# Optimization experiments

Hardware: AMD Instinct MI355X
Metric: run time of the kernel (lower is better)

Reference implementation:

```python
import jax, jax.numpy as jnp
import numpy as np

NB_HEADS = 4
EMBED_DIM = 128
EPS = 1e-06


def setup_inputs() -> dict:
    key = jax.random.key(0)
    ks = jax.random.split(key, 9)
    B, R, C, E = 2, 64, 2048, 128
    s = 1.0 / np.sqrt(E)
    inp = {
        "input": jax.random.normal(ks[0], (B, R, C, E), dtype=jnp.float32),
        # weights stored as (in, out); torch Linear applies x @ W.T + b, equivalent here
        "Wq": jax.random.normal(ks[1], (E, E), dtype=jnp.float32) * s,
        "bq": jax.random.normal(ks[2], (E,), dtype=jnp.float32) * 0.01,
        "Wk": jax.random.normal(ks[3], (E, E), dtype=jnp.float32) * s,
        "bk": jax.random.normal(ks[4], (E,), dtype=jnp.float32) * 0.01,
        "Wv": jax.random.normal(ks[5], (E, E), dtype=jnp.float32) * s,
        "bv": jax.random.normal(ks[6], (E,), dtype=jnp.float32) * 0.01,
        "Wo": jax.random.normal(ks[7], (E, E), dtype=jnp.float32) * s,
        "bo": jax.random.normal(ks[8], (E,), dtype=jnp.float32) * 0.01,
    }
    return inp


def reference(input, Wq, bq, Wk, bk, Wv, bv, Wo, bo):
    B, R, C, E = input.shape
    H = NB_HEADS
    Dh = E // H
    # projections, split into heads: (B, R, C, H, Dh)
    q = (input @ Wq + bq).reshape(B, R, C, H, Dh)
    k = (input @ Wk + bk).reshape(B, R, C, H, Dh)
    v = (input @ Wv + bv).reshape(B, R, C, H, Dh)
    # elu+1 feature map
    q = jax.nn.elu(q) + 1.0
    k = jax.nn.elu(k) + 1.0
    # KtV: contract over col axis -> (B, R, H, Dh, Dh)
    KtV = jnp.einsum('brchd,brche->brhde', k, v)
    # normalizer: q . sum_c(k) -> (B, R, C, H)
    ksum = k.sum(axis=2)  # (B, R, H, Dh)
    Z = 1.0 / (jnp.einsum('brchd,brhd->brch', q, ksum) + EPS)
    # attention output: (B, R, C, H, Dh)
    out = jnp.einsum('brchd,brhde->brche', q, KtV) * Z[..., None]
    out = out.reshape(B, R, C, E)
    return out @ Wo + bo
```

## Files before the change

kernel.cpp:

```cpp
#include <hip/hip_runtime.h>

#define DEVINL __device__ __forceinline__

typedef __attribute__((ext_vector_type(8))) __bf16 bf16x8;
typedef __attribute__((ext_vector_type(4))) __bf16 bf16x4;
typedef __attribute__((ext_vector_type(4))) float f32x4;

DEVINL f32x4 mfma16(bf16x8 a, bf16x8 b, f32x4 c) {
  return __builtin_amdgcn_mfma_f32_16x16x32_bf16(a, b, c, 0, 0, 0);
}

DEVINL bf16x8 loadWfrag(const float* __restrict__ W, int kb, int n) {
  bf16x8 f;
#pragma unroll
  for (int j = 0; j < 8; ++j) f[j] = (__bf16)W[(kb + j) * 128 + n];
  return f;
}

__global__ __launch_bounds__(256, 2)
void qkv_ktv_kernel(const float* __restrict__ X,
                    const float* __restrict__ Wq, const float* __restrict__ bq,
                    const float* __restrict__ Wk, const float* __restrict__ bk,
                    const float* __restrict__ Wv, const float* __restrict__ bv,
                    __bf16* __restrict__ Qout,
                    float* __restrict__ ktvWs, float* __restrict__ ksumWs)
{
  __shared__ __bf16 Xs[64 * 136];
  __shared__ __bf16 Kt[128 * 72];
  __shared__ __bf16 Vt[128 * 72];

  const int tid  = threadIdx.x;
  const int lane = tid & 63;
  const int w    = tid >> 6;
  const int l15  = lane & 15;
  const int quad = lane >> 4;
  const int s     = blockIdx.x >> 2;
  const int chunk = blockIdx.x & 3;
  const int tokc0 = chunk * 512;
  const float* Xseq = X + (size_t)s * 2048 * 128;

  bf16x8 wkF[2][4], wvF[2][4], wqF[2][4];
#pragma unroll
  for (int nt = 0; nt < 2; ++nt) {
    const int n = w * 32 + nt * 16 + l15;
#pragma unroll
    for (int kk = 0; kk < 4; ++kk) {
      const int kb = kk * 32 + quad * 8;
      wkF[nt][kk] = loadWfrag(Wk, kb, n);
      wvF[nt][kk] = loadWfrag(Wv, kb, n);
      wqF[nt][kk] = loadWfrag(Wq, kb, n);
    }
  }
  float bkr[2], bvr[2], bqr[2][4];
#pragma unroll
  for (int nt = 0; nt < 2; ++nt) {
    bkr[nt] = bk[w * 32 + nt * 16 + l15];
    bvr[nt] = bv[w * 32 + nt * 16 + l15];
#pragma unroll
    for (int r = 0; r < 4; ++r)
      bqr[nt][r] = bq[w * 32 + nt * 16 + quad * 4 + r];
  }

  f32x4 accT[2][2] = {};
  float ksumAcc[2] = {0.f, 0.f};

  for (int t = 0; t < 8; ++t) {
    const float* Xtile = Xseq + (size_t)(tokc0 + t * 64) * 128;
    __syncthreads();
#pragma unroll
    for (int i = 0; i < 8; ++i) {
      const int flat = tid + i * 256;
      const int row = flat >> 5;
      const int c4  = (flat & 31) * 4;
      const float4 v = *(const float4*)(Xtile + row * 128 + c4);
      bf16x4 b4;
      b4[0] = (__bf16)v.x; b4[1] = (__bf16)v.y;
      b4[2] = (__bf16)v.z; b4[3] = (__bf16)v.w;
      *(bf16x4*)(&Xs[row * 136 + c4]) = b4;
    }
    __syncthreads();

#pragma unroll
    for (int mt = 0; mt < 4; ++mt) {
      f32x4 aK[2] = {}, aV[2] = {};
#pragma unroll
      for (int kk = 0; kk < 4; ++kk) {
        const bf16x8 ax = *(const bf16x8*)(&Xs[(mt * 16 + l15) * 136 + kk * 32 + quad * 8]);
        aK[0] = mfma16(ax, wkF[0][kk], aK[0]);
        aK[1] = mfma16(ax, wkF[1][kk], aK[1]);
        aV[0] = mfma16(ax, wvF[0][kk], aV[0]);
        aV[1] = mfma16(ax, wvF[1][kk], aV[1]);
      }
#pragma unroll
      for (int nt = 0; nt < 2; ++nt) {
        const int e    = w * 32 + nt * 16 + l15;
        const int tokb = mt * 16 + quad * 4;
        bf16x4 kq, vq;
        float ks = 0.f;
#pragma unroll
        for (int r = 0; r < 4; ++r) {
          float kv = aK[nt][r] + bkr[nt];
          kv = (kv > 0.f) ? (kv + 1.f) : __expf(kv);
          ks += kv;
          kq[r] = (__bf16)kv;
          vq[r] = (__bf16)(aV[nt][r] + bvr[nt]);
        }
        ksumAcc[nt] += ks;
        *(bf16x4*)(&Kt[e * 72 + tokb]) = kq;
        *(bf16x4*)(&Vt[e * 72 + tokb]) = vq;
      }
    }

#pragma unroll
    for (int ntq = 0; ntq < 4; ++ntq) {
      f32x4 aQ[2] = {};
#pragma unroll
      for (int kk = 0; kk < 4; ++kk) {
        const bf16x8 bx = *(const bf16x8*)(&Xs[(ntq * 16 + l15) * 136 + kk * 32 + quad * 8]);
        aQ[0] = mfma16(wqF[0][kk], bx, aQ[0]);
        aQ[1] = mfma16(wqF[1][kk], bx, aQ[1]);
      }
      const int tok = tokc0 + t * 64 + ntq * 16 + l15;
      __bf16* qrow = Qout + ((size_t)s * 2048 + tok) * 128;
#pragma unroll
      for (int mt = 0; mt < 2; ++mt) {
        bf16x4 qq;
#pragma unroll
        for (int r = 0; r < 4; ++r) {
          float qv = aQ[mt][r] + bqr[mt][r];
          qv = (qv > 0.f) ? (qv + 1.f) : __expf(qv);
          qq[r] = (__bf16)qv;
        }
        *(bf16x4*)(qrow + w * 32 + mt * 16 + quad * 4) = qq;
      }
    }
    __syncthreads();

#pragma unroll
    for (int kk = 0; kk < 2; ++kk) {
      bf16x8 aF[2], bF[2];
#pragma unroll
      for (int dt = 0; dt < 2; ++dt)
        aF[dt] = *(const bf16x8*)(&Kt[(w * 32 + dt * 16 + l15) * 72 + kk * 32 + quad * 8]);
#pragma unroll
      for (int et = 0; et < 2; ++et)
        bF[et] = *(const bf16x8*)(&Vt[(w * 32 + et * 16 + l15) * 72 + kk * 32 + quad * 8]);
#pragma unroll
      for (int dt = 0; dt < 2; ++dt)
#pragma unroll
        for (int et = 0; et < 2; ++et)
          accT[dt][et] = mfma16(aF[dt], bF[et], accT[dt][et]);
    }
  }

  float* ktvH = ktvWs + ((size_t)s * 4 + w) * 1024;
#pragma unroll
  for (int dt = 0; dt < 2; ++dt)
#pragma unroll
    for (int et = 0; et < 2; ++et)
#pragma unroll
      for (int r = 0; r < 4; ++r)
        atomicAdd(&ktvH[(dt * 16 + quad * 4 + r) * 32 + et * 16 + l15], accT[dt][et][r]);

#pragma unroll
  for (int nt = 0; nt < 2; ++nt) {
    float v2 = ksumAcc[nt];
    v2 += __shfl_down(v2, 32);
    v2 += __shfl_down(v2, 16);
    if (quad == 0)
      atomicAdd(&ksumWs[s * 128 + w * 32 + nt * 16 + l15], v2);
  }
}

__global__ __launch_bounds__(256, 2)
void attn_out_kernel(const __bf16* __restrict__ Qin,
                     const float* __restrict__ ktvWs, const float* __restrict__ ksumWs,
                     const float* __restrict__ Wo, const float* __restrict__ bo,
                     float* __restrict__ Out)
{
  __shared__ __bf16 Qs[64 * 136];
  __shared__ __bf16 A2s[64 * 136];
  __shared__ float ksums[128];
  __shared__ float Zs[64 * 4];

  const int tid  = threadIdx.x;
  const int lane = tid & 63;
  const int w    = tid >> 6;
  const int l15  = lane & 15;
  const int quad = lane >> 4;
  const int s     = blockIdx.x >> 2;
  const int chunk = blockIdx.x & 3;

  if (tid < 128) ksums[tid] = ksumWs[s * 128 + tid];

  const float* ktvH = ktvWs + ((size_t)s * 4 + w) * 1024;
  bf16x8 aKtv[2];
#pragma unroll
  for (int mt = 0; mt < 2; ++mt)
#pragma unroll
    for (int j = 0; j < 8; ++j)
      aKtv[mt][j] = (__bf16)ktvH[(quad * 8 + j) * 32 + mt * 16 + l15];

  bf16x8 woF[2][4];
  float bor[2];
#pragma unroll
  for (int nt = 0; nt < 2; ++nt) {
    const int n = w * 32 + nt * 16 + l15;
    bor[nt] = bo[n];
#pragma unroll
    for (int kk = 0; kk < 4; ++kk)
      woF[nt][kk] = loadWfrag(Wo, kk * 32 + quad * 8, n);
  }
  __syncthreads();

  for (int t = 0; t < 8; ++t) {
    const int tok0 = chunk * 512 + t * 64;
    const __bf16* Qtile = Qin + ((size_t)s * 2048 + tok0) * 128;
    __syncthreads();
#pragma unroll
    for (int i = 0; i < 4; ++i) {
      const int c = tid + i * 256;
      const int row = c >> 4, cc = (c & 15) * 8;
      *(bf16x8*)(&Qs[row * 136 + cc]) = *(const bf16x8*)(Qtile + row * 128 + cc);
    }
    __syncthreads();
    {
      const int tok = tid >> 2, h = tid & 3;
      float dot = 0.f;
      const __bf16* qrow = &Qs[tok * 136 + h * 32];
      const float* ksrow = &ksums[h * 32];
#pragma unroll
      for (int j = 0; j < 32; ++j) dot += (float)qrow[j] * ksrow[j];
      Zs[tok * 4 + h] = 1.f / (dot + 1e-6f);
    }
    __syncthreads();
#pragma unroll
    for (int ntq = 0; ntq < 4; ++ntq) {
      const bf16x8 bq8 = *(const bf16x8*)(&Qs[(ntq * 16 + l15) * 136 + w * 32 + quad * 8]);
      f32x4 acc[2] = {};
      acc[0] = mfma16(aKtv[0], bq8, acc[0]);
      acc[1] = mfma16(aKtv[1], bq8, acc[1]);
      const int tokRow = ntq * 16 + l15;
      const float z = Zs[tokRow * 4 + w];
#pragma unroll
      for (int mt = 0; mt < 2; ++mt) {
        bf16x4 a4;
#pragma unroll
        for (int r = 0; r < 4; ++r) a4[r] = (__bf16)(acc[mt][r] * z);
        *(bf16x4*)(&A2s[tokRow * 136 + w * 32 + mt * 16 + quad * 4]) = a4;
      }
    }
    __syncthreads();
#pragma unroll
    for (int mt = 0; mt < 4; ++mt) {
      f32x4 acc[2] = {};
#pragma unroll
      for (int kk = 0; kk < 4; ++kk) {
        const bf16x8 aa = *(const bf16x8*)(&A2s[(mt * 16 + l15) * 136 + kk * 32 + quad * 8]);
        acc[0] = mfma16(aa, woF[0][kk], acc[0]);
        acc[1] = mfma16(aa, woF[1][kk], acc[1]);
      }
      const int tokb = tok0 + mt * 16 + quad * 4;
      float* orow = Out + ((size_t)s * 2048 + tokb) * 128;
#pragma unroll
      for (int nt = 0; nt < 2; ++nt) {
        const int n = w * 32 + nt * 16 + l15;
#pragma unroll
        for (int r = 0; r < 4; ++r)
          orow[(size_t)r * 128 + n] = acc[nt][r] + bor[nt];
      }
    }
  }
}

extern "C" void kernel_launch(void* const* d_in, const int* in_sizes, int n_in,
                              void* d_out, int out_size, void* d_ws, size_t ws_size,
                              hipStream_t stream) {
  const float* X  = (const float*)d_in[0];
  const float* Wq = (const float*)d_in[1];
  const float* bq = (const float*)d_in[2];
  const float* Wk = (const float*)d_in[3];
  const float* bk = (const float*)d_in[4];
  const float* Wv = (const float*)d_in[5];
  const float* bv = (const float*)d_in[6];
  const float* Wo = (const float*)d_in[7];
  const float* bo = (const float*)d_in[8];
  float* Out = (float*)d_out;

  const size_t Q_BYTES    = (size_t)128 * 2048 * 128 * 2;
  const size_t KTV_BYTES  = (size_t)128 * 4 * 32 * 32 * 4;
  const size_t KSUM_BYTES = (size_t)128 * 128 * 4;
  __bf16* Qws   = (__bf16*)d_ws;
  float* ktvWs  = (float*)((char*)d_ws + Q_BYTES);
  float* ksumWs = (float*)((char*)d_ws + Q_BYTES + KTV_BYTES);

  hipMemsetAsync((char*)d_ws + Q_BYTES, 0, KTV_BYTES + KSUM_BYTES, stream);

  qkv_ktv_kernel<<<dim3(512), dim3(256), 0, stream>>>(
      X, Wq, bq, Wk, bk, Wv, bv, Qws, ktvWs, ksumWs);
  attn_out_kernel<<<dim3(512), dim3(256), 0, stream>>>(
      Qws, ktvWs, ksumWs, Wo, bo, Out);
}
```

Before: 310.5 us.

## Recompute Q in output kernel instead of materializing it, split grid finer

Moves the Q projection out of the first kernel and into the output kernel, which rereads X and recomputes Q rather than writing and then reading a bf16 Q buffer in global memory. The normalizer is computed in registers with shuffles, and Q and A2 share one LDS buffer. Both kernels now launch 1024 blocks of 256 tokens with higher occupancy hints, and the first kernel register-prefetches the next X tile. The trade is a second fp32 read of X in place of the bf16 Q write and read, plus more blocks doing atomic adds into KtV.

```diff
diff --git a/kernel.cpp b/kernel.cpp
--- a/kernel.cpp
+++ b/kernel.cpp
@@ -17,13 +17,11 @@
   return f;
 }
 
-__global__ __launch_bounds__(256, 2)
-void qkv_ktv_kernel(const float* __restrict__ X,
-                    const float* __restrict__ Wq, const float* __restrict__ bq,
-                    const float* __restrict__ Wk, const float* __restrict__ bk,
-                    const float* __restrict__ Wv, const float* __restrict__ bv,
-                    __bf16* __restrict__ Qout,
-                    float* __restrict__ ktvWs, float* __restrict__ ksumWs)
+__global__ __launch_bounds__(256, 3)
+void kv_ktv_kernel(const float* __restrict__ X,
+                   const float* __restrict__ Wk, const float* __restrict__ bk,
+                   const float* __restrict__ Wv, const float* __restrict__ bv,
+                   float* __restrict__ ktvWs, float* __restrict__ ksumWs)
 {
   __shared__ __bf16 Xs[64 * 136];
   __shared__ __bf16 Kt[128 * 72];
@@ -34,12 +32,18 @@
   const int w    = tid >> 6;
   const int l15  = lane & 15;
   const int quad = lane >> 4;
-  const int s     = blockIdx.x >> 2;
-  const int chunk = blockIdx.x & 3;
-  const int tokc0 = chunk * 512;
-  const float* Xseq = X + (size_t)s * 2048 * 128;
-
-  bf16x8 wkF[2][4], wvF[2][4], wqF[2][4];
+  const int s     = blockIdx.x >> 3;
+  const int chunk = blockIdx.x & 7;
+  const float* Xc = X + ((size_t)s * 2048 + chunk * 256) * 128;
+
+  float4 xst[8];
+#pragma unroll
+  for (int i = 0; i < 8; ++i) {
+    const int flat = tid + i * 256;
+    xst[i] = *(const float4*)(Xc + (flat >> 5) * 128 + (flat & 31) * 4);
+  }
+
+  bf16x8 wkF[2][4], wvF[2][4];
 #pragma unroll
   for (int nt = 0; nt < 2; ++nt) {
     const int n = w * 32 + nt * 16 + l15;
@@ -48,35 +52,37 @@
       const int kb = kk * 32 + quad * 8;
       wkF[nt][kk] = loadWfrag(Wk, kb, n);
       wvF[nt][kk] = loadWfrag(Wv, kb, n);
-      wqF[nt][kk] = loadWfrag(Wq, kb, n);
-    }
-  }
-  float bkr[2], bvr[2], bqr[2][4];
+    }
+  }
+  float bkr[2], bvr[2];
 #pragma unroll
   for (int nt = 0; nt < 2; ++nt) {
     bkr[nt] = bk[w * 32 + nt * 16 + l15];
     bvr[nt] = bv[w * 32 + nt * 16 + l15];
-#pragma unroll
-    for (int r = 0; r < 4; ++r)
-      bqr[nt][r] = bq[w * 32 + nt * 16 + quad * 4 + r];
   }
 
   f32x4 accT[2][2] = {};
   float ksumAcc[2] = {0.f, 0.f};
 
-  for (int t = 0; t < 8; ++t) {
-    const float* Xtile = Xseq + (size_t)(tokc0 + t * 64) * 128;
+  for (int t = 0; t < 4; ++t) {
     __syncthreads();
 #pragma unroll
     for (int i = 0; i < 8; ++i) {
       const int flat = tid + i * 256;
       const int row = flat >> 5;
       const int c4  = (flat & 31) * 4;
-      const float4 v = *(const float4*)(Xtile + row * 128 + c4);
       bf16x4 b4;
-      b4[0] = (__bf16)v.x; b4[1] = (__bf16)v.y;
-      b4[2] = (__bf16)v.z; b4[3] = (__bf16)v.w;
+      b4[0] = (__bf16)xst[i].x; b4[1] = (__bf16)xst[i].y;
+      b4[2] = (__bf16)xst[i].z; b4[3] = (__bf16)xst[i].w;
       *(bf16x4*)(&Xs[row * 136 + c4]) = b4;
+    }
+    if (t < 3) {
+      const float* Xn = Xc + (t + 1) * 64 * 128;
+#pragma unroll
+      for (int i = 0; i < 8; ++i) {
+        const int flat = tid + i * 256;
+        xst[i] = *(const float4*)(Xn + (flat >> 5) * 128 + (flat & 31) * 4);
+      }
     }
     __syncthreads();
 
@@ -112,31 +118,6 @@
     }
 
 #pragma unroll
-    for (int ntq = 0; ntq < 4; ++ntq) {
-      f32x4 aQ[2] = {};
-#pragma unroll
-      for (int kk = 0; kk < 4; ++kk) {
-        const bf16x8 bx = *(const bf16x8*)(&Xs[(ntq * 16 + l15) * 136 + kk * 32 + quad * 8]);
-        aQ[0] = mfma16(wqF[0][kk], bx, aQ[0]);
-        aQ[1] = mfma16(wqF[1][kk], bx, aQ[1]);
-      }
-      const int tok = tokc0 + t * 64 + ntq * 16 + l15;
-      __bf16* qrow = Qout + ((size_t)s * 2048 + tok) * 128;
-#pragma unroll
-      for (int mt = 0; mt < 2; ++mt) {
-        bf16x4 qq;
-#pragma unroll
-        for (int r = 0; r < 4; ++r) {
-          float qv = aQ[mt][r] + bqr[mt][r];
-          qv = (qv > 0.f) ? (qv + 1.f) : __expf(qv);
-          qq[r] = (__bf16)qv;
-        }
-        *(bf16x4*)(qrow + w * 32 + mt * 16 + quad * 4) = qq;
-      }
-    }
-    __syncthreads();
-
-#pragma unroll
     for (int kk = 0; kk < 2; ++kk) {
       bf16x8 aF[2], bF[2];
 #pragma unroll
@@ -172,27 +153,43 @@
   }
 }
 
-__global__ __launch_bounds__(256, 2)
-void attn_out_kernel(const __bf16* __restrict__ Qin,
+__global__ __launch_bounds__(256, 4)
+void attn_out_kernel(const float* __restrict__ X,
+                     const float* __restrict__ Wq, const float* __restrict__ bq,
                      const float* __restrict__ ktvWs, const float* __restrict__ ksumWs,
                      const float* __restrict__ Wo, const float* __restrict__ bo,
                      float* __restrict__ Out)
 {
-  __shared__ __bf16 Qs[64 * 136];
-  __shared__ __bf16 A2s[64 * 136];
-  __shared__ float ksums[128];
-  __shared__ float Zs[64 * 4];
+  __shared__ __bf16 Xs[64 * 136];
+  __shared__ __bf16 QA2s[64 * 136];
 
   const int tid  = threadIdx.x;
   const int lane = tid & 63;
   const int w    = tid >> 6;
   const int l15  = lane & 15;
   const int quad = lane >> 4;
-  const int s     = blockIdx.x >> 2;
-  const int chunk = blockIdx.x & 3;
-
-  if (tid < 128) ksums[tid] = ksumWs[s * 128 + tid];
-
+  const int s     = blockIdx.x >> 3;
+  const int chunk = blockIdx.x & 7;
+  const float* Xc = X + ((size_t)s * 2048 + chunk * 256) * 128;
+  float* OutC = Out + ((size_t)s * 2048 + chunk * 256) * 128;
+
+  bf16x8 wqF[2][4], woF[2][4];
+  float bqr[2][4], bor[2], ksumr[2][4];
+#pragma unroll
+  for (int nt = 0; nt < 2; ++nt) {
+    const int n = w * 32 + nt * 16 + l15;
+#pragma unroll
+    for (int kk = 0; kk < 4; ++kk) {
+      wqF[nt][kk] = loadWfrag(Wq, kk * 32 + quad * 8, n);
+      woF[nt][kk] = loadWfrag(Wo, kk * 32 + quad * 8, n);
+    }
+    bor[nt] = bo[n];
+#pragma unroll
+    for (int r = 0; r < 4; ++r) {
+      bqr[nt][r]   = bq[w * 32 + nt * 16 + quad * 4 + r];
+      ksumr[nt][r] = ksumWs[s * 128 + w * 32 + nt * 16 + quad * 4 + r];
+    }
+  }
   const float* ktvH = ktvWs + ((size_t)s * 4 + w) * 1024;
   bf16x8 aKtv[2];
 #pragma unroll
@@ -201,67 +198,77 @@
     for (int j = 0; j < 8; ++j)
       aKtv[mt][j] = (__bf16)ktvH[(quad * 8 + j) * 32 + mt * 16 + l15];
 
-  bf16x8 woF[2][4];
-  float bor[2];
-#pragma unroll
-  for (int nt = 0; nt < 2; ++nt) {
-    const int n = w * 32 + nt * 16 + l15;
-    bor[nt] = bo[n];
-#pragma unroll
-    for (int kk = 0; kk < 4; ++kk)
-      woF[nt][kk] = loadWfrag(Wo, kk * 32 + quad * 8, n);
-  }
-  __syncthreads();
-
-  for (int t = 0; t < 8; ++t) {
-    const int tok0 = chunk * 512 + t * 64;
-    const __bf16* Qtile = Qin + ((size_t)s * 2048 + tok0) * 128;
-    __syncthreads();
-#pragma unroll
-    for (int i = 0; i < 4; ++i) {
-      const int c = tid + i * 256;
-      const int row = c >> 4, cc = (c & 15) * 8;
-      *(bf16x8*)(&Qs[row * 136 + cc]) = *(const bf16x8*)(Qtile + row * 128 + cc);
-    }
-    __syncthreads();
-    {
-      const int tok = tid >> 2, h = tid & 3;
+  for (int t = 0; t < 4; ++t) {
+    const float* Xt = Xc + t * 64 * 128;
+    __syncthreads();
+#pragma unroll
+    for (int i = 0; i < 8; ++i) {
+      const int flat = tid + i * 256;
+      const int row = flat >> 5;
+      const int c4  = (flat & 31) * 4;
+      const float4 v = *(const float4*)(Xt + row * 128 + c4);
+      bf16x4 b4;
+      b4[0] = (__bf16)v.x; b4[1] = (__bf16)v.y;
+      b4[2] = (__bf16)v.z; b4[3] = (__bf16)v.w;
+      *(bf16x4*)(&Xs[row * 136 + c4]) = b4;
+    }
+    __syncthreads();
+
+    float zreg[4];
+#pragma unroll
+    for (int ntq = 0; ntq < 4; ++ntq) {
+      f32x4 aQ[2] = {};
+#pragma unroll
+      for (int kk = 0; kk < 4; ++kk) {
+        const bf16x8 bx = *(const bf16x8*)(&Xs[(ntq * 16 + l15) * 136 + kk * 32 + quad * 8]);
+        aQ[0] = mfma16(wqF[0][kk], bx, aQ[0]);
+        aQ[1] = mfma16(wqF[1][kk], bx, aQ[1]);
+      }
       float dot = 0.f;
-      const __bf16* qrow = &Qs[tok * 136 + h * 32];
-      const float* ksrow = &ksums[h * 32];
-#pragma unroll
-      for (int j = 0; j < 32; ++j) dot += (float)qrow[j] * ksrow[j];
-      Zs[tok * 4 + h] = 1.f / (dot + 1e-6f);
-    }
-    __syncthreads();
+#pragma unroll
+      for (int mt = 0; mt < 2; ++mt) {
+        bf16x4 qq;
+#pragma unroll
+        for (int r = 0; r < 4; ++r) {
+          float qv = aQ[mt][r] + bqr[mt][r];
+          qv = (qv > 0.f) ? (qv + 1.f) : __expf(qv);
+          dot += qv * ksumr[mt][r];
+          qq[r] = (__bf16)qv;
+        }
+        *(bf16x4*)(&QA2s[(ntq * 16 + l15) * 136 + w * 32 + mt * 16 + quad * 4]) = qq;
+      }
+      dot += __shfl_xor(dot, 16);
+      dot += __shfl_xor(dot, 32);
+      zreg[ntq] = 1.f / (dot + 1e-6f);
+    }
+
 #pragma unroll
     for (int ntq = 0; ntq < 4; ++ntq) {
-      const bf16x8 bq8 = *(const bf16x8*)(&Qs[(ntq * 16 + l15) * 136 + w * 32 + quad * 8]);
+      const bf16x8 bq8 = *(const bf16x8*)(&QA2s[(ntq * 16 + l15) * 136 + w * 32 + quad * 8]);
       f32x4 acc[2] = {};
       acc[0] = mfma16(aKtv[0], bq8, acc[0]);
       acc[1] = mfma16(aKtv[1], bq8, acc[1]);
-      const int tokRow = ntq * 16 + l15;
-      const float z = Zs[tokRow * 4 + w];
+      const float z = zreg[ntq];
 #pragma unroll
       for (int mt = 0; mt < 2; ++mt) {
         bf16x4 a4;
 #pragma unroll
         for (int r = 0; r < 4; ++r) a4[r] = (__bf16)(acc[mt][r] * z);
-        *(bf16x4*)(&A2s[tokRow * 136 + w * 32 + mt * 16 + quad * 4]) = a4;
-      }
-    }
-    __syncthreads();
+        *(bf16x4*)(&QA2s[(ntq * 16 + l15) * 136 + w * 32 + mt * 16 + quad * 4]) = a4;
+      }
+    }
+    __syncthreads();
+
 #pragma unroll
     for (int mt = 0; mt < 4; ++mt) {
       f32x4 acc[2] = {};
 #pragma unroll
       for (int kk = 0; kk < 4; ++kk) {
-        const bf16x8 aa = *(const bf16x8*)(&A2s[(mt * 16 + l15) * 136 + kk * 32 + quad * 8]);
+        const bf16x8 aa = *(const bf16x8*)(&QA2s[(mt * 16 + l15) * 136 + kk * 32 + quad * 8]);
         acc[0] = mfma16(aa, woF[0][kk], acc[0]);
         acc[1] = mfma16(aa, woF[1][kk], acc[1]);
       }
-      const int tokb = tok0 + mt * 16 + quad * 4;
-      float* orow = Out + ((size_t)s * 2048 + tokb) * 128;
+      float* orow = OutC + (size_t)(t * 64 + mt * 16 + quad * 4) * 128;
 #pragma unroll
       for (int nt = 0; nt < 2; ++nt) {
         const int n = w * 32 + nt * 16 + l15;
@@ -287,17 +294,15 @@
   const float* bo = (const float*)d_in[8];
   float* Out = (float*)d_out;
 
-  const size_t Q_BYTES    = (size_t)128 * 2048 * 128 * 2;
   const size_t KTV_BYTES  = (size_t)128 * 4 * 32 * 32 * 4;
   const size_t KSUM_BYTES = (size_t)128 * 128 * 4;
-  __bf16* Qws   = (__bf16*)d_ws;
-  float* ktvWs  = (float*)((char*)d_ws + Q_BYTES);
-  float* ksumWs = (float*)((char*)d_ws + Q_BYTES + KTV_BYTES);
-
-  hipMemsetAsync((char*)d_ws + Q_BYTES, 0, KTV_BYTES + KSUM_BYTES, stream);
-
-  qkv_ktv_kernel<<<dim3(512), dim3(256), 0, stream>>>(
-      X, Wq, bq, Wk, bk, Wv, bv, Qws, ktvWs, ksumWs);
-  attn_out_kernel<<<dim3(512), dim3(256), 0, stream>>>(
-      Qws, ktvWs, ksumWs, Wo, bo, Out);
-}
+  float* ktvWs  = (float*)d_ws;
+  float* ksumWs = (float*)((char*)d_ws + KTV_BYTES);
+
+  hipMemsetAsync(d_ws, 0, KTV_BYTES + KSUM_BYTES, stream);
+
+  kv_ktv_kernel<<<dim3(1024), dim3(256), 0, stream>>>(
+      X, Wk, bk, Wv, bv, ktvWs, ksumWs);
+  attn_out_kernel<<<dim3(1024), dim3(256), 0, stream>>>(
+      X, Wq, bq, ktvWs, ksumWs, Wo, bo, Out);
+}
```

Result: slower. 439.0 us (+41.4%).

## Split sequences into 8 chunks with partial KtV buffers instead of atomics

Applied to the files above, without the earlier changes.

Doubles the grid to 1024 blocks of 256 tokens each and raises the launch-bounds occupancy target to 4 blocks per CU. Each block now writes its partial KtV and ksum to a private slot, and the output kernel reduces the 8 partials, which removes the memset and the global atomics. The KtV MFMA is interleaved with the K/V projection in 32-token halves using smaller LDS tiles, dropping one barrier per tile. The normalizer Z is computed in registers with shuffles instead of a separate LDS pass. In exchange, every output block re-reads and re-sums 8 partial tiles, and the higher occupancy target may cause register spills.

```diff
diff --git a/kernel.cpp b/kernel.cpp
--- a/kernel.cpp
+++ b/kernel.cpp
@@ -17,27 +17,27 @@
   return f;
 }
 
-__global__ __launch_bounds__(256, 2)
+__global__ __launch_bounds__(256, 4)
 void qkv_ktv_kernel(const float* __restrict__ X,
                     const float* __restrict__ Wq, const float* __restrict__ bq,
                     const float* __restrict__ Wk, const float* __restrict__ bk,
                     const float* __restrict__ Wv, const float* __restrict__ bv,
                     __bf16* __restrict__ Qout,
-                    float* __restrict__ ktvWs, float* __restrict__ ksumWs)
+                    float* __restrict__ ktvP, float* __restrict__ ksumP)
 {
   __shared__ __bf16 Xs[64 * 136];
-  __shared__ __bf16 Kt[128 * 72];
-  __shared__ __bf16 Vt[128 * 72];
+  __shared__ __bf16 Kt[128 * 40];
+  __shared__ __bf16 Vt[128 * 40];
 
   const int tid  = threadIdx.x;
   const int lane = tid & 63;
   const int w    = tid >> 6;
   const int l15  = lane & 15;
   const int quad = lane >> 4;
-  const int s     = blockIdx.x >> 2;
-  const int chunk = blockIdx.x & 3;
-  const int tokc0 = chunk * 512;
-  const float* Xseq = X + (size_t)s * 2048 * 128;
+  const int s     = blockIdx.x >> 3;
+  const int chunk = blockIdx.x & 7;
+  const int tokc0 = chunk * 256;
+  const float* Xc = X + ((size_t)s * 2048 + tokc0) * 128;
 
   bf16x8 wkF[2][4], wvF[2][4], wqF[2][4];
 #pragma unroll
@@ -64,8 +64,8 @@
   f32x4 accT[2][2] = {};
   float ksumAcc[2] = {0.f, 0.f};
 
-  for (int t = 0; t < 8; ++t) {
-    const float* Xtile = Xseq + (size_t)(tokc0 + t * 64) * 128;
+  for (int t = 0; t < 4; ++t) {
+    const float* Xtile = Xc + t * 64 * 128;
     __syncthreads();
 #pragma unroll
     for (int i = 0; i < 8; ++i) {
@@ -81,34 +81,50 @@
     __syncthreads();
 
 #pragma unroll
-    for (int mt = 0; mt < 4; ++mt) {
-      f32x4 aK[2] = {}, aV[2] = {};
-#pragma unroll
-      for (int kk = 0; kk < 4; ++kk) {
-        const bf16x8 ax = *(const bf16x8*)(&Xs[(mt * 16 + l15) * 136 + kk * 32 + quad * 8]);
-        aK[0] = mfma16(ax, wkF[0][kk], aK[0]);
-        aK[1] = mfma16(ax, wkF[1][kk], aK[1]);
-        aV[0] = mfma16(ax, wvF[0][kk], aV[0]);
-        aV[1] = mfma16(ax, wvF[1][kk], aV[1]);
-      }
-#pragma unroll
-      for (int nt = 0; nt < 2; ++nt) {
-        const int e    = w * 32 + nt * 16 + l15;
-        const int tokb = mt * 16 + quad * 4;
-        bf16x4 kq, vq;
-        float ks = 0.f;
-#pragma unroll
-        for (int r = 0; r < 4; ++r) {
-          float kv = aK[nt][r] + bkr[nt];
-          kv = (kv > 0.f) ? (kv + 1.f) : __expf(kv);
-          ks += kv;
-          kq[r] = (__bf16)kv;
-          vq[r] = (__bf16)(aV[nt][r] + bvr[nt]);
+    for (int half = 0; half < 2; ++half) {
+#pragma unroll
+      for (int mt2 = 0; mt2 < 2; ++mt2) {
+        const int mt = half * 2 + mt2;
+        f32x4 aK[2] = {}, aV[2] = {};
+#pragma unroll
+        for (int kk = 0; kk < 4; ++kk) {
+          const bf16x8 ax = *(const bf16x8*)(&Xs[(mt * 16 + l15) * 136 + kk * 32 + quad * 8]);
+          aK[0] = mfma16(ax, wkF[0][kk], aK[0]);
+          aK[1] = mfma16(ax, wkF[1][kk], aK[1]);
+          aV[0] = mfma16(ax, wvF[0][kk], aV[0]);
+          aV[1] = mfma16(ax, wvF[1][kk], aV[1]);
         }
-        ksumAcc[nt] += ks;
-        *(bf16x4*)(&Kt[e * 72 + tokb]) = kq;
-        *(bf16x4*)(&Vt[e * 72 + tokb]) = vq;
-      }
+#pragma unroll
+        for (int nt = 0; nt < 2; ++nt) {
+          const int e    = w * 32 + nt * 16 + l15;
+          const int tokb = mt2 * 16 + quad * 4;
+          bf16x4 kq, vq;
+          float ks = 0.f;
+#pragma unroll
+          for (int r = 0; r < 4; ++r) {
+            float kv = aK[nt][r] + bkr[nt];
+            kv = (kv > 0.f) ? (kv + 1.f) : __expf(kv);
+            ks += kv;
+            kq[r] = (__bf16)kv;
+            vq[r] = (__bf16)(aV[nt][r] + bvr[nt]);
+          }
+          ksumAcc[nt] += ks;
+          *(bf16x4*)(&Kt[e * 40 + tokb]) = kq;
+          *(bf16x4*)(&Vt[e * 40 + tokb]) = vq;
+        }
+      }
+      bf16x8 aF[2], bF[2];
+#pragma unroll
+      for (int dt = 0; dt < 2; ++dt)
+        aF[dt] = *(const bf16x8*)(&Kt[(w * 32 + dt * 16 + l15) * 40 + quad * 8]);
+#pragma unroll
+      for (int et = 0; et < 2; ++et)
+        bF[et] = *(const bf16x8*)(&Vt[(w * 32 + et * 16 + l15) * 40 + quad * 8]);
+#pragma unroll
+      for (int dt = 0; dt < 2; ++dt)
+#pragma unroll
+        for (int et = 0; et < 2; ++et)
+          accT[dt][et] = mfma16(aF[dt], bF[et], accT[dt][et]);
     }
 
 #pragma unroll
@@ -134,33 +150,16 @@
         *(bf16x4*)(qrow + w * 32 + mt * 16 + quad * 4) = qq;
       }
     }
-    __syncthreads();
-
-#pragma unroll
-    for (int kk = 0; kk < 2; ++kk) {
-      bf16x8 aF[2], bF[2];
-#pragma unroll
-      for (int dt = 0; dt < 2; ++dt)
-        aF[dt] = *(const bf16x8*)(&Kt[(w * 32 + dt * 16 + l15) * 72 + kk * 32 + quad * 8]);
-#pragma unroll
-      for (int et = 0; et < 2; ++et)
-        bF[et] = *(const bf16x8*)(&Vt[(w * 32 + et * 16 + l15) * 72 + kk * 32 + quad * 8]);
-#pragma unroll
-      for (int dt = 0; dt < 2; ++dt)
-#pragma unroll
-        for (int et = 0; et < 2; ++et)
-          accT[dt][et] = mfma16(aF[dt], bF[et], accT[dt][et]);
-    }
-  }
-
-  float* ktvH = ktvWs + ((size_t)s * 4 + w) * 1024;
+  }
+
+  float* kp = ktvP + ((size_t)blockIdx.x * 4 + w) * 1024;
 #pragma unroll
   for (int dt = 0; dt < 2; ++dt)
 #pragma unroll
     for (int et = 0; et < 2; ++et)
 #pragma unroll
       for (int r = 0; r < 4; ++r)
-        atomicAdd(&ktvH[(dt * 16 + quad * 4 + r) * 32 + et * 16 + l15], accT[dt][et][r]);
+        kp[(dt * 16 + quad * 4 + r) * 32 + et * 16 + l15] = accT[dt][et][r];
 
 #pragma unroll
   for (int nt = 0; nt < 2; ++nt) {
@@ -168,38 +167,48 @@
     v2 += __shfl_down(v2, 32);
     v2 += __shfl_down(v2, 16);
     if (quad == 0)
-      atomicAdd(&ksumWs[s * 128 + w * 32 + nt * 16 + l15], v2);
-  }
-}
-
-__global__ __launch_bounds__(256, 2)
+      ksumP[(size_t)blockIdx.x * 128 + w * 32 + nt * 16 + l15] = v2;
+  }
+}
+
+__global__ __launch_bounds__(256, 4)
 void attn_out_kernel(const __bf16* __restrict__ Qin,
-                     const float* __restrict__ ktvWs, const float* __restrict__ ksumWs,
+                     const float* __restrict__ ktvP, const float* __restrict__ ksumP,
                      const float* __restrict__ Wo, const float* __restrict__ bo,
                      float* __restrict__ Out)
 {
   __shared__ __bf16 Qs[64 * 136];
   __shared__ __bf16 A2s[64 * 136];
-  __shared__ float ksums[128];
-  __shared__ float Zs[64 * 4];
 
   const int tid  = threadIdx.x;
   const int lane = tid & 63;
   const int w    = tid >> 6;
   const int l15  = lane & 15;
   const int quad = lane >> 4;
-  const int s     = blockIdx.x >> 2;
-  const int chunk = blockIdx.x & 3;
-
-  if (tid < 128) ksums[tid] = ksumWs[s * 128 + tid];
-
-  const float* ktvH = ktvWs + ((size_t)s * 4 + w) * 1024;
+  const int s     = blockIdx.x >> 3;
+  const int chunk = blockIdx.x & 7;
+
+  const float* kpBase = ktvP + ((size_t)s * 8 * 4 + w) * 1024;
   bf16x8 aKtv[2];
 #pragma unroll
   for (int mt = 0; mt < 2; ++mt)
 #pragma unroll
-    for (int j = 0; j < 8; ++j)
-      aKtv[mt][j] = (__bf16)ktvH[(quad * 8 + j) * 32 + mt * 16 + l15];
+    for (int j = 0; j < 8; ++j) {
+      float acc = 0.f;
+#pragma unroll
+      for (int c = 0; c < 8; ++c)
+        acc += kpBase[(size_t)c * 4096 + (quad * 8 + j) * 32 + mt * 16 + l15];
+      aKtv[mt][j] = (__bf16)acc;
+    }
+  float ksum8[8];
+#pragma unroll
+  for (int j = 0; j < 8; ++j) {
+    float a = 0.f;
+#pragma unroll
+    for (int c = 0; c < 8; ++c)
+      a += ksumP[((size_t)s * 8 + c) * 128 + w * 32 + quad * 8 + j];
+    ksum8[j] = a;
+  }
 
   bf16x8 woF[2][4];
   float bor[2];
@@ -211,10 +220,9 @@
     for (int kk = 0; kk < 4; ++kk)
       woF[nt][kk] = loadWfrag(Wo, kk * 32 + quad * 8, n);
   }
-  __syncthreads();
-
-  for (int t = 0; t < 8; ++t) {
-    const int tok0 = chunk * 512 + t * 64;
+
+  for (int t = 0; t < 4; ++t) {
+    const int tok0 = chunk * 256 + t * 64;
     const __bf16* Qtile = Qin + ((size_t)s * 2048 + tok0) * 128;
     __syncthreads();
 #pragma unroll
@@ -224,33 +232,29 @@
       *(bf16x8*)(&Qs[row * 136 + cc]) = *(const bf16x8*)(Qtile + row * 128 + cc);
     }
     __syncthreads();
-    {
-      const int tok = tid >> 2, h = tid & 3;
-      float dot = 0.f;
-      const __bf16* qrow = &Qs[tok * 136 + h * 32];
-      const float* ksrow = &ksums[h * 32];
-#pragma unroll
-      for (int j = 0; j < 32; ++j) dot += (float)qrow[j] * ksrow[j];
-      Zs[tok * 4 + h] = 1.f / (dot + 1e-6f);
-    }
-    __syncthreads();
+
 #pragma unroll
     for (int ntq = 0; ntq < 4; ++ntq) {
       const bf16x8 bq8 = *(const bf16x8*)(&Qs[(ntq * 16 + l15) * 136 + w * 32 + quad * 8]);
+      float dot = 0.f;
+#pragma unroll
+      for (int j = 0; j < 8; ++j) dot += (float)bq8[j] * ksum8[j];
+      dot += __shfl_xor(dot, 16);
+      dot += __shfl_xor(dot, 32);
+      const float z = 1.f / (dot + 1e-6f);
       f32x4 acc[2] = {};
       acc[0] = mfma16(aKtv[0], bq8, acc[0]);
       acc[1] = mfma16(aKtv[1], bq8, acc[1]);
-      const int tokRow = ntq * 16 + l15;
-      const float z = Zs[tokRow * 4 + w];
 #pragma unroll
       for (int mt = 0; mt < 2; ++mt) {
         bf16x4 a4;
 #pragma unroll
         for (int r = 0; r < 4; ++r) a4[r] = (__bf16)(acc[mt][r] * z);
-        *(bf16x4*)(&A2s[tokRow * 136 + w * 32 + mt * 16 + quad * 4]) = a4;
-      }
-    }
-    __syncthreads();
+        *(bf16x4*)(&A2s[(ntq * 16 + l15) * 136 + w * 32 + mt * 16 + quad * 4]) = a4;
+      }
+    }
+    __syncthreads();
+
 #pragma unroll
     for (int mt = 0; mt < 4; ++mt) {
       f32x4 acc[2] = {};
@@ -288,16 +292,14 @@
   float* Out = (float*)d_out;
 
   const size_t Q_BYTES    = (size_t)128 * 2048 * 128 * 2;
-  const size_t KTV_BYTES  = (size_t)128 * 4 * 32 * 32 * 4;
-  const size_t KSUM_BYTES = (size_t)128 * 128 * 4;
+  const size_t KTVP_BYTES = (size_t)1024 * 4 * 1024 * 4;
   __bf16* Qws   = (__bf16*)d_ws;
-  float* ktvWs  = (float*)((char*)d_ws + Q_BYTES);
-  float* ksumWs = (float*)((char*)d_ws + Q_BYTES + KTV_BYTES);
-
-  hipMemsetAsync((char*)d_ws + Q_BYTES, 0, KTV_BYTES + KSUM_BYTES, stream);
-
-  qkv_ktv_kernel<<<dim3(512), dim3(256), 0, stream>>>(
-      X, Wq, bq, Wk, bk, Wv, bv, Qws, ktvWs, ksumWs);
-  attn_out_kernel<<<dim3(512), dim3(256), 0, stream>>>(
-      Qws, ktvWs, ksumWs, Wo, bo, Out);
-}
+  float* ktvP   = (float*)((char*)d_ws + Q_BYTES);
+  float* ksumP  = (float*)((char*)d_ws + Q_BYTES + KTVP_BYTES);
+
+
+  qkv_ktv_kernel<<<dim3(1024), dim3(256), 0, stream>>>(
+      X, Wq, bq, Wk, bk, Wv, bv, Qws, ktvP, ksumP);
+  attn_out_kernel<<<dim3(1024), dim3(256), 0, stream>>>(
+      Qws, ktvP, ksumP, Wo, bo, Out);
+}
```

Measured after the change: 471.4 us. +51.8%, slower.
